# Kernel tuning notes

Measured on AMD Instinct MI355X. Metric: run time of the kernel, lower is better.

## Reference

```python
import jax, jax.numpy as jnp
import numpy as np


def setup_inputs() -> dict:
    key = jax.random.key(0)
    k1, k2 = jax.random.split(key)
    x = jax.random.normal(k1, (16, 1, 512, 512), dtype=jnp.float32)
    weight = jax.random.normal(k2, (128, 1), dtype=jnp.float32)
    return {"x": x, "weight": weight}


def reference(x, weight):
    # x: [B, C=1, H, W]; weight: [K=128, D=1] codebook
    inputs = jnp.transpose(x, (0, 2, 3, 1))          # [B, H, W, C]
    input_shape = inputs.shape
    D = weight.shape[1]
    flat = inputs.reshape(-1, D)                     # [N, D]
    # pairwise squared distances: ||z||^2 + ||e||^2 - 2 z.e^T  -> [N, K]
    dist = (jnp.sum(flat ** 2, axis=1, keepdims=True)
            + jnp.sum(weight ** 2, axis=1)
            - 2.0 * flat @ weight.T)
    idx = jnp.argmin(dist, axis=1)                   # [N]
    # one-hot @ weight == gather of codebook rows (same math, no [N,K] one-hot)
    quantized = weight[idx].reshape(input_shape)     # [B, H, W, C]
    return jnp.transpose(quantized, (0, 3, 1, 2))    # [B, C, H, W]
```

## Files before the change

### kernel.cpp

```cpp
#include <hip/hip_runtime.h>


constexpr int K     = 128;
constexpr int EPT   = 8;
constexpr int BLOCK = 256;

__global__ __launch_bounds__(BLOCK) void vq_kernel(const float* __restrict__ x,
                                                   const float* __restrict__ w,
                                                   float* __restrict__ out,
                                                   long n, int kk) {
#pragma clang fp contract(off)
    __shared__ float  wraw[K];
    __shared__ float  sv[K];
    __shared__ float2 wp[K];
    __shared__ int    si[K];

    const int t = threadIdx.x;
    if (t < K) {
        wraw[t] = (t < kk) ? w[t] : __builtin_inff();
        sv[t]   = __builtin_inff();
        wp[t]   = make_float2(__builtin_inff(), __builtin_inff());
        si[t]   = 0x7fffffff;
    }
    __syncthreads();
    if (t < kk) {
        float v = wraw[t];
        int rank = 0;
        for (int j = 0; j < kk; ++j) {
            float u = wraw[j];
            rank += (u < v) || (u == v && j < t);
        }
        float v2 = v * v;
        asm volatile("" : "+v"(v2));
        sv[rank] = v;
        wp[rank] = make_float2(v, v2);
        si[rank] = t;
    }
    __syncthreads();

    const float m1  = sv[63];
    const float m2a = sv[31],  m2b = sv[95];
    const float m3a = sv[15],  m3b = sv[47], m3c = sv[79], m3d = sv[111];

    long base = ((long)blockIdx.x * BLOCK + t) * (long)EPT;
    if (base + EPT <= n) {
        float4 a = *(const float4*)(x + base);
        float4 b = *(const float4*)(x + base + 4);
        float xs[EPT] = {a.x, a.y, a.z, a.w, b.x, b.y, b.z, b.w};
        float res[EPT];
#pragma unroll
        for (int e = 0; e < EPT; ++e) {
            float xv = xs[e];
            float x2 = xv * xv;
            asm volatile("" : "+v"(x2));
            float tx = xv + xv;

            int pos = (m1 < xv) ? 64 : 0;
            float m2 = (pos & 64) ? m2b : m2a;
            pos += (m2 < xv) ? 32 : 0;
            float m3lo = (pos & 32) ? m3b : m3a;
            float m3hi = (pos & 32) ? m3d : m3c;
            float m3   = (pos & 64) ? m3hi : m3lo;
            pos += (m3 < xv) ? 16 : 0;
#pragma unroll
            for (int step = 8; step > 0; step >>= 1)
                pos += (sv[pos + step - 1] < xv) ? step : 0;

            int s = pos - 4;
            int smax = (kk > 8 ? kk : 8) - 8;
            s = s < 0 ? 0 : (s > smax ? smax : s);

            float best = __builtin_inff();
            int bestPos = s;
            float bw = 0.0f;
#pragma unroll
            for (int c = 0; c < 8; ++c) {
                float2 p = wp[s + c];
                float sum  = x2 + p.y;
                float prod = tx * p.x;
                asm volatile("" : "+v"(prod));
                float d = sum - prod;
                if (d < best) {
                    best = d; bestPos = s + c; bw = p.x;
                } else if (d == best) {
                    if (si[s + c] < si[bestPos]) { bestPos = s + c; bw = p.x; }
                }
            }
            res[e] = bw;
        }
        *(float4*)(out + base)     = make_float4(res[0], res[1], res[2], res[3]);
        *(float4*)(out + base + 4) = make_float4(res[4], res[5], res[6], res[7]);
    } else {
        for (long i = base; i < n; ++i) {
            float xv = x[i];
            float x2 = xv * xv;
            asm volatile("" : "+v"(x2));
            float tx = xv + xv;
            float best = __builtin_inff(), bwv = 0.0f;
            int bestIdx = 0x7fffffff;
            for (int p0 = 0; p0 < kk; ++p0) {
                float2 p = wp[p0];
                float sum  = x2 + p.y;
                float prod = tx * p.x;
                asm volatile("" : "+v"(prod));
                float d = sum - prod;
                if (d < best || (d == best && si[p0] < bestIdx)) {
                    best = d; bwv = p.x; bestIdx = si[p0];
                }
            }
            out[i] = bwv;
        }
    }
}

extern "C" void kernel_launch(void* const* d_in, const int* in_sizes, int n_in,
                              void* d_out, int out_size, void* d_ws, size_t ws_size,
                              hipStream_t stream) {
    const float* x = (const float*)d_in[0];
    const float* w = (const float*)d_in[1];
    float* out     = (float*)d_out;
    long n = (long)in_sizes[0];
    int  kk = in_sizes[1] < K ? in_sizes[1] : K;

    long threads_needed = (n + EPT - 1) / EPT;
    long grid = (threads_needed + BLOCK - 1) / BLOCK;
    vq_kernel<<<(int)grid, BLOCK, 0, stream>>>(x, w, out, n, kk);
}
```

Baseline: 81.27 us.

## Hoist fourth search level into registers, drop wp/si tables, defer ties to fallback

```diff
diff --git a/kernel.cpp b/kernel.cpp
--- a/kernel.cpp
+++ b/kernel.cpp
@@ -10,17 +10,13 @@
                                                    float* __restrict__ out,
                                                    long n, int kk) {
 #pragma clang fp contract(off)
-    __shared__ float  wraw[K];
-    __shared__ float  sv[K];
-    __shared__ float2 wp[K];
-    __shared__ int    si[K];
+    __shared__ float wraw[K];
+    __shared__ float sv[K];
 
     const int t = threadIdx.x;
     if (t < K) {
         wraw[t] = (t < kk) ? w[t] : __builtin_inff();
         sv[t]   = __builtin_inff();
-        wp[t]   = make_float2(__builtin_inff(), __builtin_inff());
-        si[t]   = 0x7fffffff;
     }
     __syncthreads();
     if (t < kk) {
@@ -30,17 +26,15 @@
             float u = wraw[j];
             rank += (u < v) || (u == v && j < t);
         }
-        float v2 = v * v;
-        asm volatile("" : "+v"(v2));
         sv[rank] = v;
-        wp[rank] = make_float2(v, v2);
-        si[rank] = t;
     }
     __syncthreads();
 
     const float m1  = sv[63];
     const float m2a = sv[31],  m2b = sv[95];
-    const float m3a = sv[15],  m3b = sv[47], m3c = sv[79], m3d = sv[111];
+    const float m3a = sv[15],  m3b = sv[47],  m3c = sv[79],  m3d = sv[111];
+    const float q0  = sv[7],   q1  = sv[23],  q2  = sv[39],  q3  = sv[55];
+    const float q4  = sv[71],  q5  = sv[87],  q6  = sv[103], q7  = sv[119];
 
     long base = ((long)blockIdx.x * BLOCK + t) * (long)EPT;
     if (base + EPT <= n) {
@@ -48,6 +42,7 @@
         float4 b = *(const float4*)(x + base + 4);
         float xs[EPT] = {a.x, a.y, a.z, a.w, b.x, b.y, b.z, b.w};
         float res[EPT];
+        int tiebits = 0;
 #pragma unroll
         for (int e = 0; e < EPT; ++e) {
             float xv = xs[e];
@@ -62,32 +57,65 @@
             float m3hi = (pos & 32) ? m3d : m3c;
             float m3   = (pos & 64) ? m3hi : m3lo;
             pos += (m3 < xv) ? 16 : 0;
-#pragma unroll
-            for (int step = 8; step > 0; step >>= 1)
-                pos += (sv[pos + step - 1] < xv) ? step : 0;
+            float u0 = (pos & 16) ? q1 : q0;
+            float u1 = (pos & 16) ? q3 : q2;
+            float u2 = (pos & 16) ? q5 : q4;
+            float u3 = (pos & 16) ? q7 : q6;
+            float v0 = (pos & 32) ? u1 : u0;
+            float v1 = (pos & 32) ? u3 : u2;
+            float m4 = (pos & 64) ? v1 : v0;
+            pos += (m4 < xv) ? 8 : 0;
+            pos += (sv[pos + 3] < xv) ? 4 : 0;
+            pos += (sv[pos + 1] < xv) ? 2 : 0;
+            pos += (sv[pos]     < xv) ? 1 : 0;
 
             int s = pos - 4;
-            int smax = (kk > 8 ? kk : 8) - 8;
-            s = s < 0 ? 0 : (s > smax ? smax : s);
+            s = s < 0 ? 0 : (s > K - 8 ? K - 8 : s);
 
             float best = __builtin_inff();
-            int bestPos = s;
-            float bw = 0.0f;
+            float bw   = 0.0f;
+            bool  tie  = false;
 #pragma unroll
             for (int c = 0; c < 8; ++c) {
-                float2 p = wp[s + c];
-                float sum  = x2 + p.y;
-                float prod = tx * p.x;
+                float wv = sv[s + c];
+                float w2 = wv * wv;
+                asm volatile("" : "+v"(w2));
+                float sum  = x2 + w2;
+                float prod = tx * wv;
                 asm volatile("" : "+v"(prod));
                 float d = sum - prod;
-                if (d < best) {
-                    best = d; bestPos = s + c; bw = p.x;
-                } else if (d == best) {
-                    if (si[s + c] < si[bestPos]) { bestPos = s + c; bw = p.x; }
-                }
+                bool lt = d < best;
+                bool eq = (!lt) && (d == best);
+                tie  = lt ? false : (tie || eq);
+                best = lt ? d  : best;
+                bw   = lt ? wv : bw;
             }
+            tiebits |= tie ? (1 << e) : 0;
             res[e] = bw;
         }
+
+        if (__builtin_expect(__any(tiebits != 0), 0)) {
+            for (int e = 0; e < EPT; ++e) {
+                if (!(tiebits & (1 << e))) continue;
+                float xv = xs[e];
+                float x2 = xv * xv;
+                asm volatile("" : "+v"(x2));
+                float tx = xv + xv;
+                float best = __builtin_inff(), bwv = 0.0f;
+                for (int k = 0; k < kk; ++k) {
+                    float wv = wraw[k];
+                    float w2 = wv * wv;
+                    asm volatile("" : "+v"(w2));
+                    float sum  = x2 + w2;
+                    float prod = tx * wv;
+                    asm volatile("" : "+v"(prod));
+                    float d = sum - prod;
+                    if (d < best) { best = d; bwv = wv; }
+                }
+                res[e] = bwv;
+            }
+        }
+
         *(float4*)(out + base)     = make_float4(res[0], res[1], res[2], res[3]);
         *(float4*)(out + base + 4) = make_float4(res[4], res[5], res[6], res[7]);
     } else {
@@ -97,16 +125,15 @@
             asm volatile("" : "+v"(x2));
             float tx = xv + xv;
             float best = __builtin_inff(), bwv = 0.0f;
-            int bestIdx = 0x7fffffff;
-            for (int p0 = 0; p0 < kk; ++p0) {
-                float2 p = wp[p0];
-                float sum  = x2 + p.y;
-                float prod = tx * p.x;
+            for (int k = 0; k < kk; ++k) {
+                float wv = wraw[k];
+                float w2 = wv * wv;
+                asm volatile("" : "+v"(w2));
+                float sum  = x2 + w2;
+                float prod = tx * wv;
                 asm volatile("" : "+v"(prod));
                 float d = sum - prod;
-                if (d < best || (d == best && si[p0] < bestIdx)) {
-                    best = d; bwv = p.x; bestIdx = si[p0];
-                }
+                if (d < best) { best = d; bwv = wv; }
             }
             out[i] = bwv;
         }
```

Result: slower. 112.1 us (+38.0%).
